# Kernel tuning notes

Hardware: AMD Instinct MI355X
Metric: run time of the kernel (lower is better)

## Reference

```python
import jax, jax.numpy as jnp
import numpy as np

BLOCK = 7          # hardcoded block_size
NUM_HEADS = 32     # CLIP RN50 attnpool heads
OUT_DIM = 512      # attnpool output dim == text feature dim
VOTE_CH = 512      # hardcoded channel count of `result`
NUM_BUCKETS = 6
_BOUNDS = jnp.array([8, 15, 22, 29, 36])  # class-index -> bucket boundaries from the if/elif chain


def _forward(image_features, text_features, pos_embed, q_w, q_b, k_w, k_b, v_w, v_b, out_w, out_b):
    B, C, Hf, Wf = image_features.shape
    Ho, Wo = Hf - BLOCK + 1, Wf - BLOCK + 1
    dt = image_features.dtype
    # --- batched extraction of all 7x7 sliding windows (replaces the i,j Python loop) ---
    ii = jnp.arange(Ho)[:, None] + jnp.arange(BLOCK)   # [Ho,7]
    jj = jnp.arange(Wo)[:, None] + jnp.arange(BLOCK)   # [Wo,7]
    rows = image_features[:, :, ii, :]                 # [B,C,Ho,7,Wf]
    pat = rows[:, :, :, :, jj]                         # [B,C,Ho,7,Wo,7]
    # row-major (di,dj) token order matches x.flatten(2) in CLIP AttentionPool2d
    tokens = pat.transpose(0, 2, 4, 3, 5, 1).reshape(B, Ho * Wo, BLOCK * BLOCK, C)  # [B,P,49,C]
    # --- CLIP AttentionPool2d, batched over all windows ---
    x = jnp.concatenate([tokens.mean(axis=2, keepdims=True), tokens], axis=2) + pos_embed  # [B,P,50,C]
    P, T = x.shape[1], x.shape[2]
    hd = C // NUM_HEADS
    q = (x[:, :, :1] @ q_w.T + q_b).reshape(B, P, 1, NUM_HEADS, hd)   # query = mean token
    k = (x @ k_w.T + k_b).reshape(B, P, T, NUM_HEADS, hd)
    v = (x @ v_w.T + v_b).reshape(B, P, T, NUM_HEADS, hd)
    attn = jax.nn.softmax(jnp.einsum('bpqhd,bpkhd->bphqk', q, k) * (float(hd) ** -0.5), axis=-1)
    pooled = jnp.einsum('bphqk,bpkhd->bpqhd', attn, v).reshape(B, P, C) @ out_w.T + out_b  # [B,P,512]
    # F.normalize followed by an extra /= norm (idempotent, kept for faithfulness)
    f = pooled / jnp.maximum(jnp.linalg.norm(pooled, axis=-1, keepdims=True), 1e-12)
    f = f / jnp.linalg.norm(f, axis=-1, keepdims=True)
    txt = text_features / jnp.linalg.norm(text_features, axis=-1, keepdims=True)
    logits = 100.0 * (f @ txt.T)                        # softmax is monotone -> argmax(logits)==argmax(probs)
    idx = jnp.argmax(logits, axis=-1)                   # [B,P]
    bucket = jnp.searchsorted(_BOUNDS, idx, side='right')  # 6-way grouping per the if/elif chain
    onehot = jax.nn.one_hot(bucket, NUM_BUCKETS, dtype=dt).reshape(B, Ho, Wo, NUM_BUCKETS).transpose(0, 3, 1, 2)
    # vote scatter-add (+1 over each 7x7 window) == full cross-correlation with a ones kernel
    kern = jnp.ones((NUM_BUCKETS, 1, BLOCK, BLOCK), dt)
    votes = jax.lax.conv_general_dilated(onehot, kern, (1, 1), [(BLOCK - 1, BLOCK - 1)] * 2,
                                         dimension_numbers=('NCHW', 'OIHW', 'NCHW'),
                                         feature_group_count=NUM_BUCKETS)  # [B,6,Hf,Wf]
    max_idx = jnp.argmax(votes, axis=1).astype(dt)      # torch.max returns first max index; argmax matches
    # `result` is re-created inside the per-image loop, so only slot B-1 survives (faithful to original)
    result = jnp.zeros((B, VOTE_CH, Hf, Wf), dt).at[B - 1].set(
        jnp.broadcast_to(max_idx[B - 1][None], (VOTE_CH, Hf, Wf)))
    return result / jnp.maximum(jnp.linalg.norm(result, axis=1, keepdims=True), 1e-12)


def setup_inputs() -> dict:
    key = jax.random.key(0)
    ks = jax.random.split(key, 8)
    B, C, Hf, Wf, NT = 2, 2048, 24, 24, 45
    w = lambda k, s: jax.random.normal(k, s, jnp.float32) * 0.02
    return {
        'image_features': jax.random.normal(ks[0], (B, C, Hf, Wf), jnp.float32),
        'text_features': jax.random.normal(ks[1], (NT, OUT_DIM), jnp.float32),
        'pos_embed': w(ks[2], (BLOCK * BLOCK + 1, C)),
        'q_w': w(ks[3], (C, C)), 'q_b': jnp.zeros((C,), jnp.float32),
        'k_w': w(ks[4], (C, C)), 'k_b': jnp.zeros((C,), jnp.float32),
        'v_w': w(ks[5], (C, C)), 'v_b': jnp.zeros((C,), jnp.float32),
        'out_w': w(ks[6], (OUT_DIM, C)), 'out_b': jnp.zeros((OUT_DIM,), jnp.float32),
    }


def reference(image_features, text_features, pos_embed, q_w, q_b, k_w, k_b, v_w, v_b, out_w, out_b):
    return _forward(image_features, text_features, pos_embed, q_w, q_b, k_w, k_b, v_w, v_b, out_w, out_b)
```

## Files before the change

kernel.cpp:

```cpp
#include <hip/hip_runtime.h>
#include <math.h>

#define CDIM 2048
#define HF 24
#define WF 24
#define PIX 576
#define HO 18
#define WO 18
#define NP 324
#define NHEAD 32
#define HD 64
#define NTOK 50
#define NTXT 45
#define OUTD 512
#define NKV 626
#define HJ (NHEAD * NTXT)
#define NROWS 640

typedef __attribute__((ext_vector_type(8))) short short8;
typedef __attribute__((ext_vector_type(4))) float f32x4;
typedef __attribute__((address_space(1))) const void as1c_void;
typedef __attribute__((address_space(3))) void as3_void;

__device__ inline unsigned bf16rn(float x) {
    unsigned u = __float_as_uint(x);
    return (u + 0x7FFFu + ((u >> 16) & 1u)) >> 16;
}
__device__ inline float bf16tof(unsigned h) { return __uint_as_float(h << 16); }

__device__ inline size_t frag_off(int row, int k) {
    return (size_t)(((row >> 4) * 64 + (k >> 5)) * 512)
         + (size_t)(((k & 31) >> 3) * 128 + (row & 15) * 8 + (k & 7));
}

__global__ __launch_bounds__(256) void split_w_k(
    const float* __restrict__ kw, const float* __restrict__ vw, const float* __restrict__ qw,
    ushort* __restrict__ WhK, ushort* __restrict__ WlK,
    ushort* __restrict__ WhV, ushort* __restrict__ WlV,
    ushort* __restrict__ WhQ, ushort* __restrict__ WlQ) {
    int gw = blockIdx.x * 4 + (threadIdx.x >> 6);
    int lane = threadIdx.x & 63;
    int sel = gw >> 13;
    int tl = gw & 8191;
    int m16 = tl >> 6;
    int kt = tl & 63;
    const float* src = sel == 0 ? kw : sel == 1 ? vw : qw;
    ushort* dh = sel == 0 ? WhK : sel == 1 ? WhV : WhQ;
    ushort* dl = sel == 0 ? WlK : sel == 1 ? WlV : WlQ;

    int row = m16 * 16 + (lane & 15);
    int k = kt * 32 + (lane >> 4) * 8;
    const float* sp = src + (size_t)row * CDIM + k;
    float4 a = *(const float4*)sp;
    float4 b = *(const float4*)(sp + 4);
    float xs[8] = {a.x, a.y, a.z, a.w, b.x, b.y, b.z, b.w};
    short8 hv, lv;
#pragma unroll
    for (int i = 0; i < 8; ++i) {
        unsigned hh = bf16rn(xs[i]);
        hv[i] = (short)hh;
        lv[i] = (short)bf16rn(xs[i] - bf16tof(hh));
    }
    size_t to = (size_t)tl * 512 + lane * 8;
    *(short8*)(dh + to) = hv;
    *(short8*)(dl + to) = lv;
}

__global__ __launch_bounds__(256) void splitx_k(const float* __restrict__ feat1,
                                                const float* __restrict__ pos,
                                                ushort* __restrict__ Xh, ushort* __restrict__ Xl) {
    int b = blockIdx.x, tid = threadIdx.x;
    if (b < 288) {
        __shared__ float tile[64][65];
        int n0 = (b % 9) * 64, c0 = (b / 9) * 64;
#pragma unroll
        for (int i = 0; i < 16; ++i) {
            int idx = tid + i * 256;
            int cc = idx >> 6, nn = idx & 63;
            tile[cc][nn] = feat1[(size_t)(c0 + cc) * PIX + n0 + nn];
        }
        __syncthreads();
#pragma unroll
        for (int i = 0; i < 16; ++i) {
            int idx = tid + i * 256;
            int nn = idx >> 6, cc = idx & 63;
            float x = tile[cc][nn];
            unsigned hh = bf16rn(x);
            size_t fo = frag_off(n0 + nn, c0 + cc);
            Xh[fo] = (ushort)hh;
            Xl[fo] = (ushort)bf16rn(x - bf16tof(hh));
        }
    } else {
        int g = (b - 288) * 256 + tid;
        int r = g >> 9;
        int c = (g & 511) * 4;
        float4 v = make_float4(0.f, 0.f, 0.f, 0.f);
        if (r < 50) v = *(const float4*)(pos + (size_t)r * CDIM + c);
        float xs[4] = {v.x, v.y, v.z, v.w};
        ushort h[4], l[4];
#pragma unroll
        for (int i = 0; i < 4; ++i) {
            unsigned hh = bf16rn(xs[i]);
            h[i] = (ushort)hh;
            l[i] = (ushort)bf16rn(xs[i] - bf16tof(hh));
        }
        size_t fo = frag_off(576 + r, c);
        *(ushort4*)(Xh + fo) = make_ushort4(h[0], h[1], h[2], h[3]);
        *(ushort4*)(Xl + fo) = make_ushort4(l[0], l[1], l[2], l[3]);
    }
}

#define BUFB 24576
__global__ __launch_bounds__(256, 2) void gemm_bf16_k(
    const ushort* __restrict__ WhK, const ushort* __restrict__ WlK,
    const ushort* __restrict__ WhV, const ushort* __restrict__ WlV,
    const ushort* __restrict__ WhQ, const ushort* __restrict__ WlQ,
    const ushort* __restrict__ Xh, const ushort* __restrict__ Xl,
    const float* __restrict__ k_b, const float* __restrict__ v_b, const float* __restrict__ q_b,
    float* __restrict__ Kbuf, float* __restrict__ Vbuf, float* __restrict__ Qfull)
{
    __shared__ char smem[3 * BUFB];
    int z = blockIdx.z;
    const ushort* Wh = z == 0 ? WhK : z == 1 ? WhV : WhQ;
    const ushort* Wl = z == 0 ? WlK : z == 1 ? WlV : WlQ;
    const float* bias = z == 0 ? k_b : z == 1 ? v_b : q_b;
    float* out = z == 0 ? Kbuf : z == 1 ? Vbuf : Qfull;
    int m0 = blockIdx.x * 128, n0 = blockIdx.y * 64;

    int tid = threadIdx.x, wid = tid >> 6, lane = tid & 63;
    int wm = wid >> 1, wn = wid & 1;

    const char* gsrc[6];
    int ldsoff[6];
#pragma unroll
    for (int i = 0; i < 6; ++i) {
        int g = wid * 6 + i;
        const ushort* src; int r16; int off;
        if (g < 8)       { src = Wh; r16 = (m0 >> 4) + g;        off = g * 1024; }
        else if (g < 16) { src = Wl; r16 = (m0 >> 4) + (g - 8);  off = 8192 + (g - 8) * 1024; }
        else if (g < 20) { src = Xh; r16 = (n0 >> 4) + (g - 16); off = 16384 + (g - 16) * 1024; }
        else             { src = Xl; r16 = (n0 >> 4) + (g - 20); off = 20480 + (g - 20) * 1024; }
        gsrc[i] = (const char*)src + ((size_t)r16 * 64 * 1024) + lane * 16;
        ldsoff[i] = off;
    }

    f32x4 acc[4][2];
#pragma unroll
    for (int a = 0; a < 4; ++a)
#pragma unroll
        for (int b = 0; b < 2; ++b) acc[a][b] = (f32x4)0.f;

#pragma unroll
    for (int i = 0; i < 6; ++i)
        __builtin_amdgcn_global_load_lds((as1c_void*)(gsrc[i]),
                                         (as3_void*)(smem + ldsoff[i]), 16, 0, 0);
#pragma unroll
    for (int i = 0; i < 6; ++i)
        __builtin_amdgcn_global_load_lds((as1c_void*)(gsrc[i] + 1024),
                                         (as3_void*)(smem + BUFB + ldsoff[i]), 16, 0, 0);
    asm volatile("s_waitcnt vmcnt(6)" ::: "memory");
    __builtin_amdgcn_s_barrier();
    asm volatile("" ::: "memory");

    for (int t = 0; t < 64; ++t) {
        char* rbuf = smem + (t % 3) * BUFB;
        if (t < 62) {
            char* wbuf = smem + ((t + 2) % 3) * BUFB;
#pragma unroll
            for (int i = 0; i < 6; ++i)
                __builtin_amdgcn_global_load_lds((as1c_void*)(gsrc[i] + (size_t)(t + 2) * 1024),
                                                 (as3_void*)(wbuf + ldsoff[i]), 16, 0, 0);
        }

        short8 ah[4], al[4];
#pragma unroll
        for (int fm = 0; fm < 4; ++fm) {
            int s = wm * 4 + fm;
            ah[fm] = *(const short8*)(rbuf + s * 1024 + lane * 16);
            al[fm] = *(const short8*)(rbuf + 8192 + s * 1024 + lane * 16);
        }
        short8 bh[2], bl[2];
#pragma unroll
        for (int fn = 0; fn < 2; ++fn) {
            int s = wn * 2 + fn;
            bh[fn] = *(const short8*)(rbuf + 16384 + s * 1024 + lane * 16);
            bl[fn] = *(const short8*)(rbuf + 20480 + s * 1024 + lane * 16);
        }
#pragma unroll
        for (int fn = 0; fn < 2; ++fn)
#pragma unroll
            for (int fm = 0; fm < 4; ++fm) {
                acc[fm][fn] = __builtin_amdgcn_mfma_f32_16x16x32_bf16(ah[fm], bh[fn], acc[fm][fn], 0, 0, 0);
                acc[fm][fn] = __builtin_amdgcn_mfma_f32_16x16x32_bf16(ah[fm], bl[fn], acc[fm][fn], 0, 0, 0);
                acc[fm][fn] = __builtin_amdgcn_mfma_f32_16x16x32_bf16(al[fm], bh[fn], acc[fm][fn], 0, 0, 0);
            }

        if (t < 62) asm volatile("s_waitcnt vmcnt(6)" ::: "memory");
        else        asm volatile("s_waitcnt vmcnt(0)" ::: "memory");
        __builtin_amdgcn_s_barrier();
        asm volatile("" ::: "memory");
    }

#pragma unroll
    for (int fm = 0; fm < 4; ++fm) {
        int mg = m0 + wm * 64 + fm * 16 + (lane >> 4) * 4;
        float4 bv = *(const float4*)(bias + mg);
#pragma unroll
        for (int fn = 0; fn < 2; ++fn) {
            int ng = n0 + wn * 32 + fn * 16 + (lane & 15);
            f32x4 o = acc[fm][fn];
            if (ng >= PIX) { o[0] += bv.x; o[1] += bv.y; o[2] += bv.z; o[3] += bv.w; }
            *(f32x4*)(out + (size_t)ng * CDIM + mg) = o;
        }
    }
}

__global__ __launch_bounds__(256) void colmean_k(const float* __restrict__ Qfull,
                                                 float* __restrict__ cm) {
    int i = blockIdx.x;
    int c = blockIdx.y * 1024 + threadIdx.x * 4;
    float4 v[24];
#pragma unroll
    for (int x = 0; x < 24; ++x)
        v[x] = *(const float4*)(Qfull + (size_t)(i * WF + x) * CDIM + c);
#pragma unroll
    for (int j = 0; j < 18; ++j) {
        float4 s = v[j];
#pragma unroll
        for (int d = 1; d < 7; ++d) {
            s.x += v[j + d].x; s.y += v[j + d].y; s.z += v[j + d].z; s.w += v[j + d].w;
        }
        *(float4*)(cm + (size_t)(i * 18 + j) * CDIM + c) = s;
    }
}

__global__ __launch_bounds__(256) void qmean2_k(const float* __restrict__ cm,
                                                const float* __restrict__ Qfull,
                                                float* __restrict__ Qm) {
    int pj = blockIdx.x;
    int c = blockIdx.y * 1024 + threadIdx.x * 4;
    float4 p0 = *(const float4*)(Qfull + (size_t)PIX * CDIM + c);
    float4 v[24];
#pragma unroll
    for (int x = 0; x < 24; ++x)
        v[x] = *(const float4*)(cm + (size_t)(x * 18 + pj) * CDIM + c);
#pragma unroll
    for (int pi = 0; pi < 18; ++pi) {
        float4 s = v[pi];
#pragma unroll
        for (int d = 1; d < 7; ++d) {
            s.x += v[pi + d].x; s.y += v[pi + d].y; s.z += v[pi + d].z; s.w += v[pi + d].w;
        }
        float4 r;
        r.x = s.x * (1.f / 49.f) + p0.x;
        r.y = s.y * (1.f / 49.f) + p0.y;
        r.z = s.z * (1.f / 49.f) + p0.z;
        r.w = s.w * (1.f / 49.f) + p0.w;
        *(float4*)(Qm + (size_t)(pi * 18 + pj) * CDIM + c) = r;
    }
}

__global__ __launch_bounds__(256) void poss_k(const float* __restrict__ Kbuf,
                                              const float* __restrict__ Qm,
                                              float* __restrict__ POSS) {
    __shared__ float qsl[4 * HD];
    int pb = blockIdx.x * 4, h = blockIdx.y, tid = threadIdx.x;
    qsl[tid] = Qm[(size_t)(pb + (tid >> 6)) * CDIM + h * HD + (tid & 63)];
    __syncthreads();
    if (tid < 200) {
        int pp = tid / 50, t = tid % 50;
        const float* kp = Kbuf + (size_t)(PIX + t) * CDIM + h * HD;
        const float* q = &qsl[pp * HD];
        float dot = 0.f;
#pragma unroll
        for (int d = 0; d < HD; d += 4) {
            float4 kv = *(const float4*)&kp[d];
            dot += kv.x * q[d] + kv.y * q[d + 1] + kv.z * q[d + 2] + kv.w * q[d + 3];
        }
        POSS[(size_t)(pb + pp) * (NHEAD * NTOK) + h * NTOK + t] = dot;
    }
}

__global__ __launch_bounds__(256) void txtw_k(
    const float* __restrict__ txt, const float* __restrict__ out_w, const float* __restrict__ out_b,
    float* __restrict__ TW, float* __restrict__ cconst)
{
    __shared__ float ts[OUTD];
    __shared__ float red[256], redb[256];
    int j = blockIdx.x, cb = blockIdx.y, tid = threadIdx.x;

    float n2 = 0.f, db = 0.f;
    for (int o = tid; o < OUTD; o += 256) {
        float tv = txt[(size_t)j * OUTD + o];
        ts[o] = tv;
        n2 += tv * tv;
        db += tv * out_b[o];
    }
    red[tid] = n2; redb[tid] = db;
    __syncthreads();
    for (int s = 128; s > 0; s >>= 1) {
        if (tid < s) { red[tid] += red[tid + s]; redb[tid] += redb[tid + s]; }
        __syncthreads();
    }
    float inv = 1.f / sqrtf(red[0]);

    int c = cb * 256 + tid;
    float acc = 0.f;
    for (int o = 0; o < OUTD; ++o)
        acc += ts[o] * out_w[(size_t)o * CDIM + c];
    TW[(size_t)j * CDIM + c] = acc * inv;
    if (cb == 0 && tid == 0) cconst[j] = redb[0] * inv;
}

__global__ __launch_bounds__(256) void tv_k(
    const float* __restrict__ TW, const float* __restrict__ Vbuf, float* __restrict__ TV)
{
    __shared__ float TWs[NTXT * HD];
    __shared__ float Vs[8 * HD];
    int cg = blockIdx.x, h = blockIdx.y, tid = threadIdx.x;
    int c0 = cg * 8;

    for (int idx = tid; idx < NTXT * HD; idx += 256) {
        int j = idx / HD, d = idx % HD;
        TWs[idx] = TW[(size_t)j * CDIM + h * HD + d];
    }
    for (int idx = tid; idx < 8 * HD; idx += 256) {
        int c = idx / HD, d = idx % HD;
        int col = c0 + c;
        Vs[idx] = (col < NKV) ? Vbuf[(size_t)col * CDIM + h * HD + d] : 0.f;
    }
    __syncthreads();

    for (int o = tid; o < 8 * NTXT; o += 256) {
        int c = o / NTXT, j = o % NTXT;
        int col = c0 + c;
        if (col >= NKV) continue;
        float acc = 0.f;
#pragma unroll
        for (int d = 0; d < HD; d += 4) {
            float4 tw = *(const float4*)&TWs[j * HD + d];
            float4 vv = *(const float4*)&Vs[c * HD + d];
            acc += tw.x * vv.x + tw.y * vv.y + tw.z * vv.z + tw.w * vv.w;
        }
        TV[(size_t)col * HJ + h * NTXT + j] = acc;
    }
}

__global__ __launch_bounds__(384) void attn_fused_k(
    const float* __restrict__ Kbuf, const float* __restrict__ Qm,
    const float* __restrict__ TV, const float* __restrict__ POSS,
    float* __restrict__ pooledHJ)
{
    __shared__ float qs[8 * HD];
    __shared__ float scf[8][NTOK];
    __shared__ float scp[8][NTOK];
    __shared__ int win[49];

    int flat = blockIdx.x;
    int s = (flat & 7) >> 1;
    int p = (flat >> 3) * 2 + (flat & 1);
    int h0 = s * 8;
    int pi = p / WO, pj = p % WO;
    int tid = threadIdx.x;

    if (tid < 128)
        *(float4*)&qs[tid * 4] = *(const float4*)(Qm + (size_t)p * CDIM + h0 * HD + tid * 4);
    if (tid < 49)
        win[tid] = (pi + tid / 7) * WF + (pj + tid % 7);
    for (int u = tid; u < 8 * NTOK; u += 384)
        scp[u / NTOK][u % NTOK] = POSS[(size_t)p * (NHEAD * NTOK) + h0 * NTOK + u];
    __syncthreads();

    int grp = tid >> 4, gl = tid & 15;
    for (int i = 0; i < 17; ++i) {
        int pair = i * 24 + grp;
        if (pair < 392) {
            int h = pair / 49, tt = pair % 49;
            float4 kv = *(const float4*)(Kbuf + (size_t)win[tt] * CDIM + (h0 + h) * HD + gl * 4);
            float4 qv = *(const float4*)&qs[h * HD + gl * 4];
            float d = kv.x * qv.x + kv.y * qv.y + kv.z * qv.z + kv.w * qv.w;
            d += __shfl_xor(d, 1);
            d += __shfl_xor(d, 2);
            d += __shfl_xor(d, 4);
            d += __shfl_xor(d, 8);
            if (gl == 0) scf[h][tt + 1] = d;
        }
    }
    __syncthreads();

    if (tid < 128) {
        int h = grp;
        float sloc = 0.f;
#pragma unroll
        for (int i = 0; i < 4; ++i) {
            int t = gl + 16 * i;
            if (t >= 1 && t < NTOK) sloc += scf[h][t];
        }
        sloc += __shfl_xor(sloc, 1); sloc += __shfl_xor(sloc, 2);
        sloc += __shfl_xor(sloc, 4); sloc += __shfl_xor(sloc, 8);
        float s0 = sloc * (1.f / 49.f);

        float sc[4];
        float mloc = -1e30f;
#pragma unroll
        for (int i = 0; i < 4; ++i) {
            int t = gl + 16 * i;
            if (t < NTOK) {
                float base = (t == 0) ? s0 : scf[h][t];
                sc[i] = (base + scp[h][t]) * 0.125f;
                mloc = fmaxf(mloc, sc[i]);
            }
        }
        mloc = fmaxf(mloc, __shfl_xor(mloc, 1)); mloc = fmaxf(mloc, __shfl_xor(mloc, 2));
        mloc = fmaxf(mloc, __shfl_xor(mloc, 4)); mloc = fmaxf(mloc, __shfl_xor(mloc, 8));

        float ev[4];
        float eloc = 0.f;
#pragma unroll
        for (int i = 0; i < 4; ++i) {
            int t = gl + 16 * i;
            if (t < NTOK) { ev[i] = expf(sc[i] - mloc); eloc += ev[i]; }
        }
        eloc += __shfl_xor(eloc, 1); eloc += __shfl_xor(eloc, 2);
        eloc += __shfl_xor(eloc, 4); eloc += __shfl_xor(eloc, 8);
        float inv = 1.f / eloc;
#pragma unroll
        for (int i = 0; i < 4; ++i) {
            int t = gl + 16 * i;
            if (t < NTOK) scf[h][t] = ev[i] * inv;
        }
    }
    __syncthreads();

    if (tid < 360) {
        int o = s * 360 + tid;
        int hloc = tid / 45;
        const float* apr = &scf[hloc][0];
        float lacc = 0.f, macc = 0.f;
#pragma unroll 7
        for (int t = 1; t < NTOK; ++t) {
            float a = apr[t];
            float v1 = TV[(size_t)win[t - 1] * HJ + o];
            float v2 = TV[(size_t)(PIX + t) * HJ + o];
            lacc += a * (v1 + v2);
            macc += v1;
        }
        float a0 = apr[0];
        lacc += a0 * (macc * (1.f / 49.f) + TV[(size_t)PIX * HJ + o]);
        pooledHJ[(size_t)p * HJ + o] = lacc;
    }
}

__global__ __launch_bounds__(64) void finish_k(const float* __restrict__ pooledHJ,
                                               const float* __restrict__ cconst,
                                               int* __restrict__ bucket) {
    __shared__ float lg[NTXT];
    int p = blockIdx.x, lane = threadIdx.x;
    if (lane < NTXT) {
        float s = cconst[lane];
        const float* row = pooledHJ + (size_t)p * HJ;
#pragma unroll 8
        for (int h = 0; h < NHEAD; ++h) s += row[h * NTXT + lane];
        lg[lane] = s;
    }
    __syncthreads();
    if (lane == 0) {
        float best = lg[0]; int bi = 0;
        for (int j2 = 1; j2 < NTXT; ++j2)
            if (lg[j2] > best) { best = lg[j2]; bi = j2; }
        int bk = 0;
        const int bounds[5] = {8, 15, 22, 29, 36};
#pragma unroll
        for (int u = 0; u < 5; ++u) bk += (bi >= bounds[u]) ? 1 : 0;
        bucket[p] = bk;
    }
}

__global__ void votes_k(const int* __restrict__ bucket, float* __restrict__ maxval) {
    __shared__ int bk[NP];
    int tid = threadIdx.x;
    if (tid < NP) bk[tid] = bucket[tid];
    __syncthreads();
    if (tid < PIX) {
        int y = tid / WF, x = tid % WF;
        int cnt[6] = {0, 0, 0, 0, 0, 0};
        int i0 = (y - 6 < 0) ? 0 : y - 6;
        int i1 = (y > HO - 1) ? HO - 1 : y;
        int j0 = (x - 6 < 0) ? 0 : x - 6;
        int j1 = (x > WO - 1) ? WO - 1 : x;
        for (int i = i0; i <= i1; ++i)
            for (int j = j0; j <= j1; ++j)
                cnt[bk[i * WO + j]]++;
        int best = cnt[0], bi = 0;
#pragma unroll
        for (int ch = 1; ch < 6; ++ch)
            if (cnt[ch] > best) { best = cnt[ch]; bi = ch; }
        maxval[tid] = (bi > 0) ? 0.044194173824159216f : 0.f;
    }
}

__global__ void fill_k(const float* __restrict__ maxval, float* __restrict__ out) {
    int idx = blockIdx.x * 256 + threadIdx.x;
    const int HALF = OUTD * PIX;
    if (idx >= 2 * HALF) return;
    out[idx] = (idx < HALF) ? 0.f : maxval[idx % PIX];
}

extern "C" void kernel_launch(void* const* d_in, const int* in_sizes, int n_in,
                              void* d_out, int out_size, void* d_ws, size_t ws_size,
                              hipStream_t stream) {
    const float* imgf = (const float*)d_in[0];
    const float* txt  = (const float*)d_in[1];
    const float* pos  = (const float*)d_in[2];
    const float* q_w  = (const float*)d_in[3];
    const float* q_b  = (const float*)d_in[4];
    const float* k_w  = (const float*)d_in[5];
    const float* k_b  = (const float*)d_in[6];
    const float* v_w  = (const float*)d_in[7];
    const float* v_b  = (const float*)d_in[8];
    const float* o_w  = (const float*)d_in[9];
    const float* o_b  = (const float*)d_in[10];

    const float* feat1 = imgf + (size_t)1 * CDIM * PIX;

    float* ws = (float*)d_ws;
    float* Kbuf  = ws;
    float* Vbuf  = Kbuf + (size_t)NROWS * CDIM;
    float* Qfull = Vbuf + (size_t)NROWS * CDIM;
    float* Qm    = Qfull + (size_t)NROWS * CDIM;
    float* cm    = Qm + (size_t)NP * CDIM;
    float* TW    = cm + (size_t)432 * CDIM;
    float* cconst = TW + (size_t)NTXT * CDIM;
    float* TV    = cconst + 64;
    float* pooledHJ = TV + (size_t)NKV * HJ;
    float* POSS  = pooledHJ + (size_t)NP * HJ;
    int*   bucket = (int*)(POSS + (size_t)NP * NHEAD * NTOK);
    float* maxval = (float*)(bucket + NP);
    size_t foff = (size_t)(maxval + 576 - ws);
    foff = (foff + 3) & ~(size_t)3;
    ushort* WhK = (ushort*)(ws + foff);
    ushort* WlK = WhK + (size_t)CDIM * CDIM;
    ushort* WhV = WlK + (size_t)CDIM * CDIM;
    ushort* WlV = WhV + (size_t)CDIM * CDIM;
    ushort* WhQ = WlV + (size_t)CDIM * CDIM;
    ushort* WlQ = WhQ + (size_t)CDIM * CDIM;
    ushort* Xh  = WlQ + (size_t)CDIM * CDIM;
    ushort* Xl  = Xh + (size_t)NROWS * CDIM;

    split_w_k<<<dim3(6144), dim3(256), 0, stream>>>(k_w, v_w, q_w, WhK, WlK, WhV, WlV, WhQ, WlQ);
    splitx_k<<<dim3(416), dim3(256), 0, stream>>>(feat1, pos, Xh, Xl);
    gemm_bf16_k<<<dim3(16, 10, 3), dim3(256), 0, stream>>>(WhK, WlK, WhV, WlV, WhQ, WlQ,
                                                           Xh, Xl, k_b, v_b, q_b, Kbuf, Vbuf, Qfull);
    colmean_k<<<dim3(24, 2), dim3(256), 0, stream>>>(Qfull, cm);
    qmean2_k<<<dim3(18, 2), dim3(256), 0, stream>>>(cm, Qfull, Qm);
    poss_k<<<dim3(81, 32), dim3(256), 0, stream>>>(Kbuf, Qm, POSS);
    txtw_k<<<dim3(NTXT, 8), dim3(256), 0, stream>>>(txt, o_w, o_b, TW, cconst);
    tv_k<<<dim3(79, 32), dim3(256), 0, stream>>>(TW, Vbuf, TV);
    attn_fused_k<<<dim3(NP * 4), dim3(384), 0, stream>>>(Kbuf, Qm, TV, POSS, pooledHJ);
    finish_k<<<dim3(NP), dim3(64), 0, stream>>>(pooledHJ, cconst, bucket);
    votes_k<<<dim3(1), dim3(576), 0, stream>>>(bucket, maxval);
    fill_k<<<dim3(2304), dim3(256), 0, stream>>>(maxval, (float*)d_out);
}
```

Before: 193.3 us.

## Tile text-weight projection with split-K partials and fuse vote into fill

Replaces the txtw kernel, which streamed all of out_w per text row, with three kernels. The first normalises the text rows, the second computes tiled 64x64 LDS partial products over 8 output-dim chunks, and the third reduces those partials. The aim is to reuse each out_w load across all 45 text rows instead of re-reading it per row. It also folds the single-block vote kernel into the fill kernel, so each output element of the second half recomputes its vote directly; this removes one launch at the cost of redundant vote work per channel.

Result: no change. 196.3 us (+1.5%).

```diff
diff --git a/kernel.cpp b/kernel.cpp
--- a/kernel.cpp
+++ b/kernel.cpp
@@ -281,35 +281,70 @@
     }
 }
 
-__global__ __launch_bounds__(256) void txtw_k(
-    const float* __restrict__ txt, const float* __restrict__ out_w, const float* __restrict__ out_b,
-    float* __restrict__ TW, float* __restrict__ cconst)
+__global__ __launch_bounds__(256) void tnorm_k(
+    const float* __restrict__ txt, const float* __restrict__ out_b,
+    float* __restrict__ tn, float* __restrict__ cconst)
 {
-    __shared__ float ts[OUTD];
     __shared__ float red[256], redb[256];
-    int j = blockIdx.x, cb = blockIdx.y, tid = threadIdx.x;
-
-    float n2 = 0.f, db = 0.f;
-    for (int o = tid; o < OUTD; o += 256) {
-        float tv = txt[(size_t)j * OUTD + o];
-        ts[o] = tv;
-        n2 += tv * tv;
-        db += tv * out_b[o];
-    }
-    red[tid] = n2; redb[tid] = db;
+    int j = blockIdx.x, tid = threadIdx.x;
+    float t0 = txt[(size_t)j * OUTD + tid];
+    float t1 = txt[(size_t)j * OUTD + 256 + tid];
+    red[tid] = t0 * t0 + t1 * t1;
+    redb[tid] = t0 * out_b[tid] + t1 * out_b[256 + tid];
     __syncthreads();
     for (int s = 128; s > 0; s >>= 1) {
         if (tid < s) { red[tid] += red[tid + s]; redb[tid] += redb[tid + s]; }
         __syncthreads();
     }
     float inv = 1.f / sqrtf(red[0]);
-
+    tn[(size_t)j * OUTD + tid] = t0 * inv;
+    tn[(size_t)j * OUTD + 256 + tid] = t1 * inv;
+    if (tid == 0) cconst[j] = redb[0] * inv;
+}
+
+__global__ __launch_bounds__(256) void txtw_part_k(
+    const float* __restrict__ tn, const float* __restrict__ out_w,
+    float* __restrict__ Part)
+{
+    __shared__ float ws[64][65];
+    __shared__ float ts[NTXT][64];
+    int ob = blockIdx.x, cb = blockIdx.y, tid = threadIdx.x;
+    int o0 = ob * 64, c0 = cb * 64;
+
+#pragma unroll
+    for (int r = 0; r < 16; ++r) {
+        int idx = tid + r * 256;
+        int oo = idx >> 6, cc = idx & 63;
+        ws[oo][cc] = out_w[(size_t)(o0 + oo) * CDIM + c0 + cc];
+    }
+    for (int idx = tid; idx < NTXT * 64; idx += 256) {
+        int j = idx >> 6, oo = idx & 63;
+        ts[j][oo] = tn[(size_t)j * OUTD + o0 + oo];
+    }
+    __syncthreads();
+
+    int cc = tid & 63;
+    for (int j = tid >> 6; j < NTXT; j += 4) {
+        float acc = 0.f;
+#pragma unroll
+        for (int oo = 0; oo < 64; oo += 4) {
+            acc += ts[j][oo] * ws[oo][cc] + ts[j][oo + 1] * ws[oo + 1][cc]
+                 + ts[j][oo + 2] * ws[oo + 2][cc] + ts[j][oo + 3] * ws[oo + 3][cc];
+        }
+        Part[((size_t)ob * NTXT + j) * CDIM + c0 + cc] = acc;
+    }
+}
+
+__global__ __launch_bounds__(256) void txtw_red_k(
+    const float* __restrict__ Part, float* __restrict__ TW)
+{
+    int j = blockIdx.x, cb = blockIdx.y, tid = threadIdx.x;
     int c = cb * 256 + tid;
-    float acc = 0.f;
-    for (int o = 0; o < OUTD; ++o)
-        acc += ts[o] * out_w[(size_t)o * CDIM + c];
-    TW[(size_t)j * CDIM + c] = acc * inv;
-    if (cb == 0 && tid == 0) cconst[j] = redb[0] * inv;
+    float s = 0.f;
+#pragma unroll
+    for (int ob = 0; ob < 8; ++ob)
+        s += Part[((size_t)ob * NTXT + j) * CDIM + c];
+    TW[(size_t)j * CDIM + c] = s;
 }
 
 __global__ __launch_bounds__(256) void tv_k(
@@ -476,34 +511,34 @@
     }
 }
 
-__global__ void votes_k(const int* __restrict__ bucket, float* __restrict__ maxval) {
+__global__ __launch_bounds__(256) void votefill_k(const int* __restrict__ bucket,
+                                                  float* __restrict__ out) {
+    const int HALF = OUTD * PIX;
     __shared__ int bk[NP];
     int tid = threadIdx.x;
-    if (tid < NP) bk[tid] = bucket[tid];
-    __syncthreads();
-    if (tid < PIX) {
-        int y = tid / WF, x = tid % WF;
-        int cnt[6] = {0, 0, 0, 0, 0, 0};
-        int i0 = (y - 6 < 0) ? 0 : y - 6;
-        int i1 = (y > HO - 1) ? HO - 1 : y;
-        int j0 = (x - 6 < 0) ? 0 : x - 6;
-        int j1 = (x > WO - 1) ? WO - 1 : x;
-        for (int i = i0; i <= i1; ++i)
-            for (int j = j0; j <= j1; ++j)
-                cnt[bk[i * WO + j]]++;
-        int best = cnt[0], bi = 0;
-#pragma unroll
-        for (int ch = 1; ch < 6; ++ch)
-            if (cnt[ch] > best) { best = cnt[ch]; bi = ch; }
-        maxval[tid] = (bi > 0) ? 0.044194173824159216f : 0.f;
-    }
-}
-
-__global__ void fill_k(const float* __restrict__ maxval, float* __restrict__ out) {
-    int idx = blockIdx.x * 256 + threadIdx.x;
-    const int HALF = OUTD * PIX;
+    int base = blockIdx.x * 256;
+    if (base + 255 >= HALF) {
+        for (int i = tid; i < NP; i += 256) bk[i] = bucket[i];
+        __syncthreads();
+    }
+    int idx = base + tid;
     if (idx >= 2 * HALF) return;
-    out[idx] = (idx < HALF) ? 0.f : maxval[idx % PIX];
+    if (idx < HALF) { out[idx] = 0.f; return; }
+    int pix = (idx - HALF) % PIX;
+    int y = pix / WF, x = pix % WF;
+    int cnt[6] = {0, 0, 0, 0, 0, 0};
+    int i0 = (y - 6 < 0) ? 0 : y - 6;
+    int i1 = (y > HO - 1) ? HO - 1 : y;
+    int j0 = (x - 6 < 0) ? 0 : x - 6;
+    int j1 = (x > WO - 1) ? WO - 1 : x;
+    for (int i = i0; i <= i1; ++i)
+        for (int j = j0; j <= j1; ++j)
+            cnt[bk[i * WO + j]]++;
+    int best = cnt[0], bi = 0;
+#pragma unroll
+    for (int ch = 1; ch < 6; ++ch)
+        if (cnt[ch] > best) { best = cnt[ch]; bi = ch; }
+    out[idx] = (bi > 0) ? 0.044194173824159216f : 0.f;
 }
 
 extern "C" void kernel_launch(void* const* d_in, const int* in_sizes, int n_in,
@@ -531,12 +566,14 @@
     float* cm    = Qm + (size_t)NP * CDIM;
     float* TW    = cm + (size_t)432 * CDIM;
     float* cconst = TW + (size_t)NTXT * CDIM;
-    float* TV    = cconst + 64;
+    float* tn    = cconst + 64;
+    float* Part  = tn + (size_t)NTXT * OUTD;
+    float* TV    = Part + (size_t)8 * NTXT * CDIM;
     float* pooledHJ = TV + (size_t)NKV * HJ;
     float* POSS  = pooledHJ + (size_t)NP * HJ;
     int*   bucket = (int*)(POSS + (size_t)NP * NHEAD * NTOK);
-    float* maxval = (float*)(bucket + NP);
-    size_t foff = (size_t)(maxval + 576 - ws);
+    float* endf   = (float*)(bucket + NP);
+    size_t foff = (size_t)(endf - ws);
     foff = (foff + 3) & ~(size_t)3;
     ushort* WhK = (ushort*)(ws + foff);
     ushort* WlK = WhK + (size_t)CDIM * CDIM;
@@ -554,10 +591,11 @@
     colmean_k<<<dim3(24, 2), dim3(256), 0, stream>>>(Qfull, cm);
     qmean2_k<<<dim3(18, 2), dim3(256), 0, stream>>>(cm, Qfull, Qm);
     poss_k<<<dim3(81, 32), dim3(256), 0, stream>>>(Kbuf, Qm, POSS);
-    txtw_k<<<dim3(NTXT, 8), dim3(256), 0, stream>>>(txt, o_w, o_b, TW, cconst);
+    tnorm_k<<<dim3(NTXT), dim3(256), 0, stream>>>(txt, o_b, tn, cconst);
+    txtw_part_k<<<dim3(8, 32), dim3(256), 0, stream>>>(tn, o_w, Part);
+    txtw_red_k<<<dim3(NTXT, 8), dim3(256), 0, stream>>>(Part, TW);
     tv_k<<<dim3(79, 32), dim3(256), 0, stream>>>(TW, Vbuf, TV);
     attn_fused_k<<<dim3(NP * 4), dim3(384), 0, stream>>>(Kbuf, Qm, TV, POSS, pooledHJ);
     finish_k<<<dim3(NP), dim3(64), 0, stream>>>(pooledHJ, cconst, bucket);
-    votes_k<<<dim3(1), dim3(576), 0, stream>>>(bucket, maxval);
-    fill_k<<<dim3(2304), dim3(256), 0, stream>>>(maxval, (float*)d_out);
-}
+    votefill_k<<<dim3(2304), dim3(256), 0, stream>>>(bucket, (float*)d_out);
+}
```

## Project window-mean features through Q instead of averaging projected pixels; fuse votes into fill

Applied to the files above, without the earlier changes.

Computes the 7x7 window means of the raw features first (a new mfeat kernel) and feeds those 324 mean rows plus the pos row into the Q GEMM, replacing the full-pixel Q projection and the two-pass colmean/qmean kernels. The pos-embed query row is added back in poss_k and attn_fused_k when Q is loaded. This uses linearity to shrink the Q GEMM N dimension and drop two kernels. The votes and fill kernels are merged so each output element recomputes its vote, which removes a launch but repeats the vote count across 512 channels. The extra mfeat kernel with 2048 small blocks adds some cost of its own.

Result: slower. 199.7 us (+3.3%).

```diff
diff --git a/kernel.cpp b/kernel.cpp
--- a/kernel.cpp
+++ b/kernel.cpp
@@ -16,6 +16,7 @@
 #define NKV 626
 #define HJ (NHEAD * NTXT)
 #define NROWS 640
+#define NQROWS 384
 
 typedef __attribute__((ext_vector_type(8))) short short8;
 typedef __attribute__((ext_vector_type(4))) float f32x4;
@@ -66,12 +67,38 @@
     *(short8*)(dl + to) = lv;
 }
 
+__global__ __launch_bounds__(64) void mfeat_k(const float* __restrict__ feat1,
+                                              float* __restrict__ mf) {
+    __shared__ float row[PIX];
+    __shared__ float cs[24 * 18];
+    int c = blockIdx.x, tid = threadIdx.x;
+    for (int idx = tid; idx < PIX; idx += 64) row[idx] = feat1[(size_t)c * PIX + idx];
+    __syncthreads();
+    for (int idx = tid; idx < 24 * 18; idx += 64) {
+        int i = idx / 18, j = idx % 18;
+        float s = 0.f;
+#pragma unroll
+        for (int d = 0; d < 7; ++d) s += row[i * 24 + j + d];
+        cs[idx] = s;
+    }
+    __syncthreads();
+    for (int idx = tid; idx < NP; idx += 64) {
+        int pi = idx / 18, pj = idx % 18;
+        float s = 0.f;
+#pragma unroll
+        for (int d = 0; d < 7; ++d) s += cs[(pi + d) * 18 + pj];
+        mf[(size_t)c * NP + idx] = s * (1.f / 49.f);
+    }
+}
+
 __global__ __launch_bounds__(256) void splitx_k(const float* __restrict__ feat1,
                                                 const float* __restrict__ pos,
-                                                ushort* __restrict__ Xh, ushort* __restrict__ Xl) {
+                                                const float* __restrict__ mf,
+                                                ushort* __restrict__ Xh, ushort* __restrict__ Xl,
+                                                ushort* __restrict__ Xmh, ushort* __restrict__ Xml) {
+    __shared__ float tile[64][65];
     int b = blockIdx.x, tid = threadIdx.x;
     if (b < 288) {
-        __shared__ float tile[64][65];
         int n0 = (b % 9) * 64, c0 = (b / 9) * 64;
 #pragma unroll
         for (int i = 0; i < 16; ++i) {
@@ -90,7 +117,7 @@
             Xh[fo] = (ushort)hh;
             Xl[fo] = (ushort)bf16rn(x - bf16tof(hh));
         }
-    } else {
+    } else if (b < 416) {
         int g = (b - 288) * 256 + tid;
         int r = g >> 9;
         int c = (g & 511) * 4;
@@ -107,6 +134,31 @@
         size_t fo = frag_off(576 + r, c);
         *(ushort4*)(Xh + fo) = make_ushort4(h[0], h[1], h[2], h[3]);
         *(ushort4*)(Xl + fo) = make_ushort4(l[0], l[1], l[2], l[3]);
+    } else {
+        int bb = b - 416;
+        int n0 = (bb % 6) * 64, c0 = (bb / 6) * 64;
+#pragma unroll
+        for (int i = 0; i < 16; ++i) {
+            int idx = tid + i * 256;
+            int cc = idx >> 6, nn = idx & 63;
+            int p = n0 + nn;
+            float v;
+            if (p < NP)       v = mf[(size_t)(c0 + cc) * NP + p];
+            else if (p == NP) v = pos[(size_t)0 * CDIM + c0 + cc];
+            else              v = 0.f;
+            tile[cc][nn] = v;
+        }
+        __syncthreads();
+#pragma unroll
+        for (int i = 0; i < 16; ++i) {
+            int idx = tid + i * 256;
+            int nn = idx >> 6, cc = idx & 63;
+            float x = tile[cc][nn];
+            unsigned hh = bf16rn(x);
+            size_t fo = frag_off(n0 + nn, c0 + cc);
+            Xmh[fo] = (ushort)hh;
+            Xml[fo] = (ushort)bf16rn(x - bf16tof(hh));
+        }
     }
 }
 
@@ -116,15 +168,20 @@
     const ushort* __restrict__ WhV, const ushort* __restrict__ WlV,
     const ushort* __restrict__ WhQ, const ushort* __restrict__ WlQ,
     const ushort* __restrict__ Xh, const ushort* __restrict__ Xl,
+    const ushort* __restrict__ Xmh, const ushort* __restrict__ Xml,
     const float* __restrict__ k_b, const float* __restrict__ v_b, const float* __restrict__ q_b,
-    float* __restrict__ Kbuf, float* __restrict__ Vbuf, float* __restrict__ Qfull)
+    float* __restrict__ Kbuf, float* __restrict__ Vbuf, float* __restrict__ Qm)
 {
     __shared__ char smem[3 * BUFB];
     int z = blockIdx.z;
+    if (z == 2 && blockIdx.y >= 6) return;
     const ushort* Wh = z == 0 ? WhK : z == 1 ? WhV : WhQ;
     const ushort* Wl = z == 0 ? WlK : z == 1 ? WlV : WlQ;
+    const ushort* BH = (z == 2) ? Xmh : Xh;
+    const ushort* BL = (z == 2) ? Xml : Xl;
     const float* bias = z == 0 ? k_b : z == 1 ? v_b : q_b;
-    float* out = z == 0 ? Kbuf : z == 1 ? Vbuf : Qfull;
+    float* out = z == 0 ? Kbuf : z == 1 ? Vbuf : Qm;
+    int bias_start = (z == 2) ? NP : PIX;
     int m0 = blockIdx.x * 128, n0 = blockIdx.y * 64;
 
     int tid = threadIdx.x, wid = tid >> 6, lane = tid & 63;
@@ -138,8 +195,8 @@
         const ushort* src; int r16; int off;
         if (g < 8)       { src = Wh; r16 = (m0 >> 4) + g;        off = g * 1024; }
         else if (g < 16) { src = Wl; r16 = (m0 >> 4) + (g - 8);  off = 8192 + (g - 8) * 1024; }
-        else if (g < 20) { src = Xh; r16 = (n0 >> 4) + (g - 16); off = 16384 + (g - 16) * 1024; }
-        else             { src = Xl; r16 = (n0 >> 4) + (g - 20); off = 20480 + (g - 20) * 1024; }
+        else if (g < 20) { src = BH; r16 = (n0 >> 4) + (g - 16); off = 16384 + (g - 16) * 1024; }
+        else             { src = BL; r16 = (n0 >> 4) + (g - 20); off = 20480 + (g - 20) * 1024; }
         gsrc[i] = (const char*)src + ((size_t)r16 * 64 * 1024) + lane * 16;
         ldsoff[i] = off;
     }
@@ -209,54 +266,9 @@
         for (int fn = 0; fn < 2; ++fn) {
             int ng = n0 + wn * 32 + fn * 16 + (lane & 15);
             f32x4 o = acc[fm][fn];
-            if (ng >= PIX) { o[0] += bv.x; o[1] += bv.y; o[2] += bv.z; o[3] += bv.w; }
+            if (ng >= bias_start) { o[0] += bv.x; o[1] += bv.y; o[2] += bv.z; o[3] += bv.w; }
             *(f32x4*)(out + (size_t)ng * CDIM + mg) = o;
         }
-    }
-}
-
-__global__ __launch_bounds__(256) void colmean_k(const float* __restrict__ Qfull,
-                                                 float* __restrict__ cm) {
-    int i = blockIdx.x;
-    int c = blockIdx.y * 1024 + threadIdx.x * 4;
-    float4 v[24];
-#pragma unroll
-    for (int x = 0; x < 24; ++x)
-        v[x] = *(const float4*)(Qfull + (size_t)(i * WF + x) * CDIM + c);
-#pragma unroll
-    for (int j = 0; j < 18; ++j) {
-        float4 s = v[j];
-#pragma unroll
-        for (int d = 1; d < 7; ++d) {
-            s.x += v[j + d].x; s.y += v[j + d].y; s.z += v[j + d].z; s.w += v[j + d].w;
-        }
-        *(float4*)(cm + (size_t)(i * 18 + j) * CDIM + c) = s;
-    }
-}
-
-__global__ __launch_bounds__(256) void qmean2_k(const float* __restrict__ cm,
-                                                const float* __restrict__ Qfull,
-                                                float* __restrict__ Qm) {
-    int pj = blockIdx.x;
-    int c = blockIdx.y * 1024 + threadIdx.x * 4;
-    float4 p0 = *(const float4*)(Qfull + (size_t)PIX * CDIM + c);
-    float4 v[24];
-#pragma unroll
-    for (int x = 0; x < 24; ++x)
-        v[x] = *(const float4*)(cm + (size_t)(x * 18 + pj) * CDIM + c);
-#pragma unroll
-    for (int pi = 0; pi < 18; ++pi) {
-        float4 s = v[pi];
-#pragma unroll
-        for (int d = 1; d < 7; ++d) {
-            s.x += v[pi + d].x; s.y += v[pi + d].y; s.z += v[pi + d].z; s.w += v[pi + d].w;
-        }
-        float4 r;
-        r.x = s.x * (1.f / 49.f) + p0.x;
-        r.y = s.y * (1.f / 49.f) + p0.y;
-        r.z = s.z * (1.f / 49.f) + p0.z;
-        r.w = s.w * (1.f / 49.f) + p0.w;
-        *(float4*)(Qm + (size_t)(pi * 18 + pj) * CDIM + c) = r;
     }
 }
 
@@ -265,7 +277,8 @@
                                               float* __restrict__ POSS) {
     __shared__ float qsl[4 * HD];
     int pb = blockIdx.x * 4, h = blockIdx.y, tid = threadIdx.x;
-    qsl[tid] = Qm[(size_t)(pb + (tid >> 6)) * CDIM + h * HD + (tid & 63)];
+    qsl[tid] = Qm[(size_t)(pb + (tid >> 6)) * CDIM + h * HD + (tid & 63)]
+             + Qm[(size_t)NP * CDIM + h * HD + (tid & 63)];
     __syncthreads();
     if (tid < 200) {
         int pp = tid / 50, t = tid % 50;
@@ -363,8 +376,12 @@
     int pi = p / WO, pj = p % WO;
     int tid = threadIdx.x;
 
-    if (tid < 128)
-        *(float4*)&qs[tid * 4] = *(const float4*)(Qm + (size_t)p * CDIM + h0 * HD + tid * 4);
+    if (tid < 128) {
+        float4 a = *(const float4*)(Qm + (size_t)p * CDIM + h0 * HD + tid * 4);
+        float4 b = *(const float4*)(Qm + (size_t)NP * CDIM + h0 * HD + tid * 4);
+        a.x += b.x; a.y += b.y; a.z += b.z; a.w += b.w;
+        *(float4*)&qs[tid * 4] = a;
+    }
     if (tid < 49)
         win[tid] = (pi + tid / 7) * WF + (pj + tid % 7);
     for (int u = tid; u < 8 * NTOK; u += 384)
@@ -476,34 +493,34 @@
     }
 }
 
-__global__ void votes_k(const int* __restrict__ bucket, float* __restrict__ maxval) {
+__global__ __launch_bounds__(256) void votefill_k(const int* __restrict__ bucket,
+                                                  float* __restrict__ out) {
+    const int HALF = OUTD * PIX;
     __shared__ int bk[NP];
     int tid = threadIdx.x;
-    if (tid < NP) bk[tid] = bucket[tid];
-    __syncthreads();
-    if (tid < PIX) {
-        int y = tid / WF, x = tid % WF;
-        int cnt[6] = {0, 0, 0, 0, 0, 0};
-        int i0 = (y - 6 < 0) ? 0 : y - 6;
-        int i1 = (y > HO - 1) ? HO - 1 : y;
-        int j0 = (x - 6 < 0) ? 0 : x - 6;
-        int j1 = (x > WO - 1) ? WO - 1 : x;
-        for (int i = i0; i <= i1; ++i)
-            for (int j = j0; j <= j1; ++j)
-                cnt[bk[i * WO + j]]++;
-        int best = cnt[0], bi = 0;
-#pragma unroll
-        for (int ch = 1; ch < 6; ++ch)
-            if (cnt[ch] > best) { best = cnt[ch]; bi = ch; }
-        maxval[tid] = (bi > 0) ? 0.044194173824159216f : 0.f;
-    }
-}
-
-__global__ void fill_k(const float* __restrict__ maxval, float* __restrict__ out) {
-    int idx = blockIdx.x * 256 + threadIdx.x;
-    const int HALF = OUTD * PIX;
+    int base = blockIdx.x * 256;
+    if (base + 255 >= HALF) {
+        for (int i = tid; i < NP; i += 256) bk[i] = bucket[i];
+        __syncthreads();
+    }
+    int idx = base + tid;
     if (idx >= 2 * HALF) return;
-    out[idx] = (idx < HALF) ? 0.f : maxval[idx % PIX];
+    if (idx < HALF) { out[idx] = 0.f; return; }
+    int pix = (idx - HALF) % PIX;
+    int y = pix / WF, x = pix % WF;
+    int cnt[6] = {0, 0, 0, 0, 0, 0};
+    int i0 = (y - 6 < 0) ? 0 : y - 6;
+    int i1 = (y > HO - 1) ? HO - 1 : y;
+    int j0 = (x - 6 < 0) ? 0 : x - 6;
+    int j1 = (x > WO - 1) ? WO - 1 : x;
+    for (int i = i0; i <= i1; ++i)
+        for (int j = j0; j <= j1; ++j)
+            cnt[bk[i * WO + j]]++;
+    int best = cnt[0], bi = 0;
+#pragma unroll
+    for (int ch = 1; ch < 6; ++ch)
+        if (cnt[ch] > best) { best = cnt[ch]; bi = ch; }
+    out[idx] = (bi > 0) ? 0.044194173824159216f : 0.f;
 }
 
 extern "C" void kernel_launch(void* const* d_in, const int* in_sizes, int n_in,
@@ -526,17 +543,16 @@
     float* ws = (float*)d_ws;
     float* Kbuf  = ws;
     float* Vbuf  = Kbuf + (size_t)NROWS * CDIM;
-    float* Qfull = Vbuf + (size_t)NROWS * CDIM;
-    float* Qm    = Qfull + (size_t)NROWS * CDIM;
-    float* cm    = Qm + (size_t)NP * CDIM;
-    float* TW    = cm + (size_t)432 * CDIM;
+    float* Qm    = Vbuf + (size_t)NROWS * CDIM;
+    float* mf    = Qm + (size_t)NQROWS * CDIM;
+    float* TW    = mf + (size_t)CDIM * NP;
     float* cconst = TW + (size_t)NTXT * CDIM;
     float* TV    = cconst + 64;
     float* pooledHJ = TV + (size_t)NKV * HJ;
     float* POSS  = pooledHJ + (size_t)NP * HJ;
     int*   bucket = (int*)(POSS + (size_t)NP * NHEAD * NTOK);
-    float* maxval = (float*)(bucket + NP);
-    size_t foff = (size_t)(maxval + 576 - ws);
+    float* endf   = (float*)(bucket + NP);
+    size_t foff = (size_t)(endf - ws);
     foff = (foff + 3) & ~(size_t)3;
     ushort* WhK = (ushort*)(ws + foff);
     ushort* WlK = WhK + (size_t)CDIM * CDIM;
@@ -546,18 +562,19 @@
     ushort* WlQ = WhQ + (size_t)CDIM * CDIM;
     ushort* Xh  = WlQ + (size_t)CDIM * CDIM;
     ushort* Xl  = Xh + (size_t)NROWS * CDIM;
+    ushort* Xmh = Xl + (size_t)NROWS * CDIM;
+    ushort* Xml = Xmh + (size_t)NQROWS * CDIM;
 
     split_w_k<<<dim3(6144), dim3(256), 0, stream>>>(k_w, v_w, q_w, WhK, WlK, WhV, WlV, WhQ, WlQ);
-    splitx_k<<<dim3(416), dim3(256), 0, stream>>>(feat1, pos, Xh, Xl);
+    mfeat_k<<<dim3(CDIM), dim3(64), 0, stream>>>(feat1, mf);
+    splitx_k<<<dim3(608), dim3(256), 0, stream>>>(feat1, pos, mf, Xh, Xl, Xmh, Xml);
     gemm_bf16_k<<<dim3(16, 10, 3), dim3(256), 0, stream>>>(WhK, WlK, WhV, WlV, WhQ, WlQ,
-                                                           Xh, Xl, k_b, v_b, q_b, Kbuf, Vbuf, Qfull);
-    colmean_k<<<dim3(24, 2), dim3(256), 0, stream>>>(Qfull, cm);
-    qmean2_k<<<dim3(18, 2), dim3(256), 0, stream>>>(cm, Qfull, Qm);
+                                                           Xh, Xl, Xmh, Xml,
+                                                           k_b, v_b, q_b, Kbuf, Vbuf, Qm);
     poss_k<<<dim3(81, 32), dim3(256), 0, stream>>>(Kbuf, Qm, POSS);
     txtw_k<<<dim3(NTXT, 8), dim3(256), 0, stream>>>(txt, o_w, o_b, TW, cconst);
     tv_k<<<dim3(79, 32), dim3(256), 0, stream>>>(TW, Vbuf, TV);
     attn_fused_k<<<dim3(NP * 4), dim3(384), 0, stream>>>(Kbuf, Qm, TV, POSS, pooledHJ);
     finish_k<<<dim3(NP), dim3(64), 0, stream>>>(pooledHJ, cconst, bucket);
-    votes_k<<<dim3(1), dim3(576), 0, stream>>>(bucket, maxval);
-    fill_k<<<dim3(2304), dim3(256), 0, stream>>>(maxval, (float*)d_out);
-}
+    votefill_k<<<dim3(2304), dim3(256), 0, stream>>>(bucket, (float*)d_out);
+}
```
